# Optimization experiments

Hardware: AMD Instinct MI355X
Metric: run time of the kernel (lower is better)

## Reference

```python
import jax, jax.numpy as jnp
import numpy as np

R = 24  # voxel resolution
EPS = 0.0


def setup_inputs() -> dict:
    key = jax.random.key(0)
    pts = jax.random.normal(key, (32, 131072, 6), dtype=jnp.float32)
    return {"pts": pts}


def reference(pts):
    B, N, C = pts.shape
    coords = jax.lax.stop_gradient(pts[:, :, :3])            # [B,N,3] (detached in torch)
    feats = jnp.concatenate(
        [jnp.ones((B, N, 1), dtype=pts.dtype), pts[:, :, 3:]], axis=-1
    )                                                         # [B,N,4]

    # normalize coords into [0,1] per cloud
    nc = coords - coords.mean(axis=1, keepdims=True)          # [B,N,3]
    norm = jnp.linalg.norm(nc, axis=-1, keepdims=True)        # [B,N,1]
    max_norm = norm.max(axis=1, keepdims=True)                # [B,1,1]
    nc = nc / (max_norm * 2.0 + EPS) + 0.5

    nc = jnp.clip(nc * R, 0.0, R - 1)
    vox = jnp.round(nc).astype(jnp.int32)                     # [B,N,3]

    # flat voxel index with batch offset
    vidx = vox[..., 0] * R * R + vox[..., 1] * R + vox[..., 2]            # [B,N]
    flat_idx = (vidx + jnp.arange(B, dtype=jnp.int32)[:, None] * (R ** 3)).reshape(-1)

    F = feats.shape[-1]
    sums = jax.ops.segment_sum(feats.reshape(B * N, F), flat_idx,
                               num_segments=B * R ** 3)        # [B*R^3, F]
    cnts = jax.ops.segment_sum(jnp.ones((B * N,), dtype=pts.dtype), flat_idx,
                               num_segments=B * R ** 3)        # [B*R^3]
    avg = jnp.where(cnts[:, None] > 0, sums / jnp.maximum(cnts[:, None], 1.0), 0.0)

    out = avg.reshape(B, R, R, R, F)                           # [B,R,R,R,F]
    return jnp.transpose(out, (0, 4, 1, 2, 3))                 # [B,F,R,R,R]
```

## Files before the change

### kernel.cpp

```cpp
#include <hip/hip_runtime.h>

#define BATCH 32
#define NPTS 131072
#define RES 24
#define R3 (RES*RES*RES)
#define NCHUNK 8
#define CPTS (NPTS/NCHUNK)
#define NBLK_PER_B 64
#define MCHUNK (NPTS/NBLK_PER_B)
#define NSCAT (BATCH*NCHUNK)

#define QSCALE 128.0f
#define QBIAS 1024

#define WS_PARTIAL 0
#define WS_MEAN    49152
#define WS_MAXSQ   49920
#define WS_ACCUM   65536
#define PRIV_BYTES ((size_t)NSCAT * R3 * sizeof(unsigned long long))
#define SHARED_BYTES ((size_t)BATCH * R3 * 2 * sizeof(unsigned long long))

__global__ __launch_bounds__(256) void k_mean(const float* __restrict__ pts,
                                              double* __restrict__ partial) {
    int blk = blockIdx.x;
    int b = blk >> 6, c = blk & 63;
    const float4* base = (const float4*)(pts + ((size_t)b * NPTS + (size_t)c * MCHUNK) * 6);
    double s0 = 0, s1 = 0, s2 = 0;
    for (int i = threadIdx.x; i < MCHUNK / 2; i += 256) {
        float4 v0 = base[(size_t)i * 3];
        float4 v1 = base[(size_t)i * 3 + 1];
        float4 v2 = base[(size_t)i * 3 + 2];
        s0 += (double)v0.x + (double)v1.z;
        s1 += (double)v0.y + (double)v1.w;
        s2 += (double)v0.z + (double)v2.x;
    }
    for (int off = 32; off; off >>= 1) {
        s0 += __shfl_down(s0, off);
        s1 += __shfl_down(s1, off);
        s2 += __shfl_down(s2, off);
    }
    __shared__ double sh[4][3];
    int lane = threadIdx.x & 63, w = threadIdx.x >> 6;
    if (lane == 0) { sh[w][0] = s0; sh[w][1] = s1; sh[w][2] = s2; }
    __syncthreads();
    if (threadIdx.x == 0) {
        double t0 = 0, t1 = 0, t2 = 0;
        for (int q = 0; q < 4; q++) { t0 += sh[q][0]; t1 += sh[q][1]; t2 += sh[q][2]; }
        partial[(size_t)blk * 3 + 0] = t0;
        partial[(size_t)blk * 3 + 1] = t1;
        partial[(size_t)blk * 3 + 2] = t2;
    }
}

__global__ __launch_bounds__(64) void k_meanred(const double* __restrict__ partial,
                                                double* __restrict__ mean) {
    int b = threadIdx.x;
    if (b >= BATCH) return;
    double t0 = 0, t1 = 0, t2 = 0;
    for (int c = 0; c < NBLK_PER_B; c++) {
        const double* p = partial + ((size_t)b * NBLK_PER_B + c) * 3;
        t0 += p[0]; t1 += p[1]; t2 += p[2];
    }
    mean[b * 3 + 0] = t0 / (double)NPTS;
    mean[b * 3 + 1] = t1 / (double)NPTS;
    mean[b * 3 + 2] = t2 / (double)NPTS;
}

__global__ __launch_bounds__(256) void k_max(const float* __restrict__ pts,
                                             const double* __restrict__ mean,
                                             unsigned long long* __restrict__ maxsq) {
    int blk = blockIdx.x;
    int b = blk >> 6, c = blk & 63;
    double mx = mean[b * 3], my = mean[b * 3 + 1], mz = mean[b * 3 + 2];
    const float4* base = (const float4*)(pts + ((size_t)b * NPTS + (size_t)c * MCHUNK) * 6);
    double m = 0.0;
    for (int i = threadIdx.x; i < MCHUNK / 2; i += 256) {
        float4 v0 = base[(size_t)i * 3];
        float4 v1 = base[(size_t)i * 3 + 1];
        float4 v2 = base[(size_t)i * 3 + 2];
        double dx = (double)v0.x - mx, dy = (double)v0.y - my, dz = (double)v0.z - mz;
        m = fmax(m, dx * dx + dy * dy + dz * dz);
        dx = (double)v1.z - mx; dy = (double)v1.w - my; dz = (double)v2.x - mz;
        m = fmax(m, dx * dx + dy * dy + dz * dz);
    }
    for (int off = 32; off; off >>= 1)
        m = fmax(m, __shfl_down(m, off));
    __shared__ double sh[4];
    int lane = threadIdx.x & 63, w = threadIdx.x >> 6;
    if (lane == 0) sh[w] = m;
    __syncthreads();
    if (threadIdx.x == 0) {
        double t = fmax(fmax(sh[0], sh[1]), fmax(sh[2], sh[3]));
        atomicMax(&maxsq[b], (unsigned long long)__double_as_longlong(t));
    }
}

template <bool ATOMIC>
__global__ __launch_bounds__(1024, 4) void k_scatter_lds(const float* __restrict__ pts,
                                                         const double* __restrict__ mean,
                                                         const unsigned long long* __restrict__ maxsq,
                                                         unsigned long long* __restrict__ accum) {
    __shared__ unsigned long long acc[R3];
    int blk = blockIdx.x;
    int b = blk >> 3;
    int ch = blk & 7;
    for (int c = threadIdx.x; c < R3; c += 1024)
        acc[c] = 0ull;
    __syncthreads();

    double mx = mean[b * 3], my = mean[b * 3 + 1], mz = mean[b * 3 + 2];
    double inv = 1.0 / (2.0 * sqrt(__longlong_as_double((long long)maxsq[b])));

    const float4* base = (const float4*)(pts + ((size_t)b * NPTS + (size_t)ch * CPTS) * 6);

    auto point = [&](float x, float y, float z, float f1, float f2, float f3) {
        double vx = fma((double)x - mx, inv, 0.5) * 24.0;
        double vy = fma((double)y - my, inv, 0.5) * 24.0;
        double vz = fma((double)z - mz, inv, 0.5) * 24.0;
        vx = fmin(fmax(vx, 0.0), 23.0);
        vy = fmin(fmax(vy, 0.0), 23.0);
        vz = fmin(fmax(vz, 0.0), 23.0);
        int qx = (int)rint(vx);
        int qy = (int)rint(vy);
        int qz = (int)rint(vz);
        int cell = qx * (RES * RES) + qy * RES + qz;
        unsigned q1 = (unsigned)((int)rintf(f1 * QSCALE) + QBIAS);
        unsigned q2 = (unsigned)((int)rintf(f2 * QSCALE) + QBIAS);
        unsigned q3 = (unsigned)((int)rintf(f3 * QSCALE) + QBIAS);
        unsigned long long v = 1ull | ((unsigned long long)q1 << 10)
                                    | ((unsigned long long)q2 << 28)
                                    | ((unsigned long long)q3 << 46);
        atomicAdd(&acc[cell], v);
    };

    for (int it = 0; it < 2; ++it) {
        int pr = it * 4096 + threadIdx.x;
        float4 a0 = base[(size_t)pr * 3];
        float4 a1 = base[(size_t)pr * 3 + 1];
        float4 a2 = base[(size_t)pr * 3 + 2];
        float4 b0 = base[(size_t)(pr + 1024) * 3];
        float4 b1 = base[(size_t)(pr + 1024) * 3 + 1];
        float4 b2 = base[(size_t)(pr + 1024) * 3 + 2];
        float4 c0 = base[(size_t)(pr + 2048) * 3];
        float4 c1 = base[(size_t)(pr + 2048) * 3 + 1];
        float4 c2 = base[(size_t)(pr + 2048) * 3 + 2];
        float4 d0 = base[(size_t)(pr + 3072) * 3];
        float4 d1 = base[(size_t)(pr + 3072) * 3 + 1];
        float4 d2 = base[(size_t)(pr + 3072) * 3 + 2];
        point(a0.x, a0.y, a0.z, a0.w, a1.x, a1.y);
        point(a1.z, a1.w, a2.x, a2.y, a2.z, a2.w);
        point(b0.x, b0.y, b0.z, b0.w, b1.x, b1.y);
        point(b1.z, b1.w, b2.x, b2.y, b2.z, b2.w);
        point(c0.x, c0.y, c0.z, c0.w, c1.x, c1.y);
        point(c1.z, c1.w, c2.x, c2.y, c2.z, c2.w);
        point(d0.x, d0.y, d0.z, d0.w, d1.x, d1.y);
        point(d1.z, d1.w, d2.x, d2.y, d2.z, d2.w);
    }
    __syncthreads();

    if (ATOMIC) {
        for (int c = threadIdx.x; c < R3; c += 1024) {
            unsigned long long v = acc[c];
            if (v != 0ull) {
                unsigned long long cnt = v & 1023ull;
                unsigned long long g1 = (v >> 10) & 0x3FFFFull;
                unsigned long long g2 = (v >> 28) & 0x3FFFFull;
                unsigned long long g3 = (v >> 46);
                atomicAdd(&accum[((size_t)b * R3 + c) * 2 + 0], cnt | (g1 << 32));
                atomicAdd(&accum[((size_t)b * R3 + c) * 2 + 1], g2 | (g3 << 32));
            }
        }
    } else {
        ulonglong2* gacc = (ulonglong2*)(accum + (size_t)blk * R3);
        const ulonglong2* lacc = (const ulonglong2*)acc;
        for (int c = threadIdx.x; c < R3 / 2; c += 1024)
            gacc[c] = lacc[c];
    }
}

__device__ __forceinline__ void decode_write(long long cnt, long long s1, long long s2,
                                             long long s3, float* out, size_t obase) {
    if (cnt > 0) {
        float invc = 1.0f / (QSCALE * (float)cnt);
        out[obase]          = 1.0f;
        out[obase + R3]     = (float)(s1 - cnt * QBIAS) * invc;
        out[obase + 2 * R3] = (float)(s2 - cnt * QBIAS) * invc;
        out[obase + 3 * R3] = (float)(s3 - cnt * QBIAS) * invc;
    } else {
        out[obase]          = 0.0f;
        out[obase + R3]     = 0.0f;
        out[obase + 2 * R3] = 0.0f;
        out[obase + 3 * R3] = 0.0f;
    }
}

__global__ __launch_bounds__(256) void k_final_priv(const unsigned long long* __restrict__ accum,
                                                    float* __restrict__ out) {
    int cell = blockIdx.x * 256 + threadIdx.x;
    int b = cell / R3;
    int r = cell - b * R3;
    long long cnt = 0, s1 = 0, s2 = 0, s3 = 0;
    #pragma unroll
    for (int ch = 0; ch < NCHUNK; ch++) {
        unsigned long long v = accum[(size_t)(b * NCHUNK + ch) * R3 + r];
        cnt += (long long)(v & 1023ull);
        s1  += (long long)((v >> 10) & 0x3FFFFull);
        s2  += (long long)((v >> 28) & 0x3FFFFull);
        s3  += (long long)(v >> 46);
    }
    decode_write(cnt, s1, s2, s3, out, (size_t)b * 4 * R3 + r);
}

__global__ __launch_bounds__(256) void k_final_sum(const unsigned long long* __restrict__ accum,
                                                   float* __restrict__ out) {
    int cell = blockIdx.x * 256 + threadIdx.x;
    const ulonglong2 v = ((const ulonglong2*)accum)[cell];
    int b = cell / R3;
    int r = cell - b * R3;
    long long cnt = (long long)(v.x & 0xffffffffull);
    long long s1 = (long long)(v.x >> 32);
    long long s2 = (long long)(v.y & 0xffffffffull);
    long long s3 = (long long)(v.y >> 32);
    decode_write(cnt, s1, s2, s3, out, (size_t)b * 4 * R3 + r);
}

extern "C" void kernel_launch(void* const* d_in, const int* in_sizes, int n_in,
                              void* d_out, int out_size, void* d_ws, size_t ws_size,
                              hipStream_t stream) {
    const float* pts = (const float*)d_in[0];
    float* out = (float*)d_out;
    char* ws = (char*)d_ws;
    double* partial = (double*)(ws + WS_PARTIAL);
    double* mean = (double*)(ws + WS_MEAN);
    unsigned long long* maxsq = (unsigned long long*)(ws + WS_MAXSQ);
    unsigned long long* accum = (unsigned long long*)(ws + WS_ACCUM);
    bool priv = ws_size >= (size_t)WS_ACCUM + PRIV_BYTES;

    if (priv) {
        hipMemsetAsync(ws + WS_MAXSQ, 0, BATCH * sizeof(unsigned long long), stream);
    } else {
        hipMemsetAsync(ws + WS_MAXSQ, 0, (WS_ACCUM - WS_MAXSQ) + SHARED_BYTES, stream);
    }

    k_mean<<<BATCH * NBLK_PER_B, 256, 0, stream>>>(pts, partial);
    k_meanred<<<1, 64, 0, stream>>>(partial, mean);
    k_max<<<BATCH * NBLK_PER_B, 256, 0, stream>>>(pts, mean, maxsq);
    if (priv) {
        k_scatter_lds<false><<<NSCAT, 1024, 0, stream>>>(pts, mean, maxsq, accum);
        k_final_priv<<<(BATCH * R3) / 256, 256, 0, stream>>>(accum, out);
    } else {
        k_scatter_lds<true><<<NSCAT, 1024, 0, stream>>>(pts, mean, maxsq, accum);
        k_final_sum<<<(BATCH * R3) / 256, 256, 0, stream>>>(accum, out);
    }
}
```

Before: 78.51 us.

## Fuse mean, max, scatter and finalize into one cooperative kernel

Replaces the five-launch pipeline (mean, mean reduce, max, LDS scatter, finalize) with a single cooperative kernel of 256 blocks of 1024 threads that uses grid-wide syncs between stages. Each block reads its own chunk of points for the mean, the max-norm and the scatter passes, so re-reads of the same chunk may hit in cache, and the kernel-launch gaps are removed. In exchange, the mean and max passes now run on 256 large blocks instead of 2048 small ones, which lowers parallelism, and the four grid syncs add overhead. The design also depends on all 256 blocks being resident at once.

```diff
diff --git a/kernel.cpp b/kernel.cpp
--- a/kernel.cpp
+++ b/kernel.cpp
@@ -1,4 +1,7 @@
 #include <hip/hip_runtime.h>
+#include <hip/hip_cooperative_groups.h>
+
+namespace cg = cooperative_groups;
 
 #define BATCH 32
 #define NPTS 131072
@@ -6,9 +9,10 @@
 #define R3 (RES*RES*RES)
 #define NCHUNK 8
 #define CPTS (NPTS/NCHUNK)
+#define NBLOCKS (BATCH*NCHUNK)
+#define CELLS_PER_BLK ((BATCH*R3)/NBLOCKS)
 #define NBLK_PER_B 64
 #define MCHUNK (NPTS/NBLK_PER_B)
-#define NSCAT (BATCH*NCHUNK)
 
 #define QSCALE 128.0f
 #define QBIAS 1024
@@ -17,8 +21,181 @@
 #define WS_MEAN    49152
 #define WS_MAXSQ   49920
 #define WS_ACCUM   65536
-#define PRIV_BYTES ((size_t)NSCAT * R3 * sizeof(unsigned long long))
+#define PRIV_BYTES ((size_t)NBLOCKS * R3 * sizeof(unsigned long long))
 #define SHARED_BYTES ((size_t)BATCH * R3 * 2 * sizeof(unsigned long long))
+
+__device__ __forceinline__ void decode_write(long long cnt, long long s1, long long s2,
+                                             long long s3, float* out, size_t obase) {
+    if (cnt > 0) {
+        float invc = 1.0f / (QSCALE * (float)cnt);
+        out[obase]          = 1.0f;
+        out[obase + R3]     = (float)(s1 - cnt * QBIAS) * invc;
+        out[obase + 2 * R3] = (float)(s2 - cnt * QBIAS) * invc;
+        out[obase + 3 * R3] = (float)(s3 - cnt * QBIAS) * invc;
+    } else {
+        out[obase]          = 0.0f;
+        out[obase + R3]     = 0.0f;
+        out[obase + 2 * R3] = 0.0f;
+        out[obase + 3 * R3] = 0.0f;
+    }
+}
+
+__global__ __launch_bounds__(1024, 4) void k_fused(const float* __restrict__ pts,
+                                                   double* __restrict__ partial,
+                                                   double* __restrict__ mean,
+                                                   unsigned long long* __restrict__ maxsq,
+                                                   unsigned long long* __restrict__ accum,
+                                                   float* __restrict__ out) {
+    __shared__ unsigned long long acc[R3];
+    __shared__ double shred[16][3];
+    cg::grid_group grid = cg::this_grid();
+
+    const int blk = blockIdx.x;
+    const int b = blk >> 3, ch = blk & 7;
+    const int tid = threadIdx.x;
+    const int lane = tid & 63, w = tid >> 6;
+    const float4* base = (const float4*)(pts + ((size_t)b * NPTS + (size_t)ch * CPTS) * 6);
+
+    {
+        double s0 = 0, s1 = 0, s2 = 0;
+        for (int it = 0; it < 8; ++it) {
+            int pr = it * 1024 + tid;
+            float4 v0 = base[(size_t)pr * 3];
+            float4 v1 = base[(size_t)pr * 3 + 1];
+            float4 v2 = base[(size_t)pr * 3 + 2];
+            s0 += (double)v0.x + (double)v1.z;
+            s1 += (double)v0.y + (double)v1.w;
+            s2 += (double)v0.z + (double)v2.x;
+        }
+        for (int off = 32; off; off >>= 1) {
+            s0 += __shfl_down(s0, off);
+            s1 += __shfl_down(s1, off);
+            s2 += __shfl_down(s2, off);
+        }
+        if (lane == 0) { shred[w][0] = s0; shred[w][1] = s1; shred[w][2] = s2; }
+        __syncthreads();
+        if (tid == 0) {
+            double t0 = 0, t1 = 0, t2 = 0;
+            for (int q = 0; q < 16; q++) { t0 += shred[q][0]; t1 += shred[q][1]; t2 += shred[q][2]; }
+            partial[blk * 3 + 0] = t0;
+            partial[blk * 3 + 1] = t1;
+            partial[blk * 3 + 2] = t2;
+        }
+    }
+    grid.sync();
+
+    if (tid == 0 && ch == 0) {
+        double t0 = 0, t1 = 0, t2 = 0;
+        for (int c = 0; c < NCHUNK; c++) {
+            const double* p = partial + (size_t)(b * NCHUNK + c) * 3;
+            t0 += p[0]; t1 += p[1]; t2 += p[2];
+        }
+        mean[b * 3 + 0] = t0 / (double)NPTS;
+        mean[b * 3 + 1] = t1 / (double)NPTS;
+        mean[b * 3 + 2] = t2 / (double)NPTS;
+    }
+    grid.sync();
+
+    const double mx = mean[b * 3], my = mean[b * 3 + 1], mz = mean[b * 3 + 2];
+
+    {
+        double m = 0.0;
+        for (int it = 0; it < 8; ++it) {
+            int pr = it * 1024 + tid;
+            float4 v0 = base[(size_t)pr * 3];
+            float4 v1 = base[(size_t)pr * 3 + 1];
+            float4 v2 = base[(size_t)pr * 3 + 2];
+            double dx = (double)v0.x - mx, dy = (double)v0.y - my, dz = (double)v0.z - mz;
+            m = fmax(m, dx * dx + dy * dy + dz * dz);
+            dx = (double)v1.z - mx; dy = (double)v1.w - my; dz = (double)v2.x - mz;
+            m = fmax(m, dx * dx + dy * dy + dz * dz);
+        }
+        for (int off = 32; off; off >>= 1)
+            m = fmax(m, __shfl_down(m, off));
+        if (lane == 0) shred[w][0] = m;
+        __syncthreads();
+        if (tid == 0) {
+            double t = shred[0][0];
+            for (int q = 1; q < 16; q++) t = fmax(t, shred[q][0]);
+            atomicMax(&maxsq[b], (unsigned long long)__double_as_longlong(t));
+        }
+    }
+    grid.sync();
+
+    {
+        const double inv = 1.0 / (2.0 * sqrt(__longlong_as_double((long long)maxsq[b])));
+        for (int c = tid; c < R3; c += 1024)
+            acc[c] = 0ull;
+        __syncthreads();
+
+        auto point = [&](float x, float y, float z, float f1, float f2, float f3) {
+            double vx = fma((double)x - mx, inv, 0.5) * 24.0;
+            double vy = fma((double)y - my, inv, 0.5) * 24.0;
+            double vz = fma((double)z - mz, inv, 0.5) * 24.0;
+            vx = fmin(fmax(vx, 0.0), 23.0);
+            vy = fmin(fmax(vy, 0.0), 23.0);
+            vz = fmin(fmax(vz, 0.0), 23.0);
+            int qx = (int)rint(vx);
+            int qy = (int)rint(vy);
+            int qz = (int)rint(vz);
+            int cell = qx * (RES * RES) + qy * RES + qz;
+            unsigned q1 = (unsigned)((int)rintf(f1 * QSCALE) + QBIAS);
+            unsigned q2 = (unsigned)((int)rintf(f2 * QSCALE) + QBIAS);
+            unsigned q3 = (unsigned)((int)rintf(f3 * QSCALE) + QBIAS);
+            unsigned long long v = 1ull | ((unsigned long long)q1 << 10)
+                                        | ((unsigned long long)q2 << 28)
+                                        | ((unsigned long long)q3 << 46);
+            atomicAdd(&acc[cell], v);
+        };
+
+        for (int it = 0; it < 2; ++it) {
+            int pr = it * 4096 + tid;
+            float4 a0 = base[(size_t)pr * 3];
+            float4 a1 = base[(size_t)pr * 3 + 1];
+            float4 a2 = base[(size_t)pr * 3 + 2];
+            float4 b0 = base[(size_t)(pr + 1024) * 3];
+            float4 b1 = base[(size_t)(pr + 1024) * 3 + 1];
+            float4 b2 = base[(size_t)(pr + 1024) * 3 + 2];
+            float4 c0 = base[(size_t)(pr + 2048) * 3];
+            float4 c1 = base[(size_t)(pr + 2048) * 3 + 1];
+            float4 c2 = base[(size_t)(pr + 2048) * 3 + 2];
+            float4 d0 = base[(size_t)(pr + 3072) * 3];
+            float4 d1 = base[(size_t)(pr + 3072) * 3 + 1];
+            float4 d2 = base[(size_t)(pr + 3072) * 3 + 2];
+            point(a0.x, a0.y, a0.z, a0.w, a1.x, a1.y);
+            point(a1.z, a1.w, a2.x, a2.y, a2.z, a2.w);
+            point(b0.x, b0.y, b0.z, b0.w, b1.x, b1.y);
+            point(b1.z, b1.w, b2.x, b2.y, b2.z, b2.w);
+            point(c0.x, c0.y, c0.z, c0.w, c1.x, c1.y);
+            point(c1.z, c1.w, c2.x, c2.y, c2.z, c2.w);
+            point(d0.x, d0.y, d0.z, d0.w, d1.x, d1.y);
+            point(d1.z, d1.w, d2.x, d2.y, d2.z, d2.w);
+        }
+        __syncthreads();
+
+        ulonglong2* gacc = (ulonglong2*)(accum + (size_t)blk * R3);
+        const ulonglong2* lacc = (const ulonglong2*)acc;
+        for (int c = tid; c < R3 / 2; c += 1024)
+            gacc[c] = lacc[c];
+    }
+    grid.sync();
+
+    for (int i = tid; i < CELLS_PER_BLK; i += 1024) {
+        int cell = blk * CELLS_PER_BLK + i;
+        int bb = cell / R3;
+        int r = cell - bb * R3;
+        long long cnt = 0, s1 = 0, s2 = 0, s3 = 0;
+        #pragma unroll
+        for (int c2 = 0; c2 < NCHUNK; c2++) {
+            unsigned long long v = accum[(size_t)(bb * NCHUNK + c2) * R3 + r];
+            cnt += (long long)(v & 1023ull);
+            s1  += (long long)((v >> 10) & 0x3FFFFull);
+            s2  += (long long)((v >> 28) & 0x3FFFFull);
+            s3  += (long long)(v >> 46);
+        }
+        decode_write(cnt, s1, s2, s3, out, (size_t)bb * 4 * R3 + r);
+    }
+}
 
 __global__ __launch_bounds__(256) void k_mean(const float* __restrict__ pts,
                                               double* __restrict__ partial) {
@@ -95,11 +272,10 @@
     }
 }
 
-template <bool ATOMIC>
-__global__ __launch_bounds__(1024, 4) void k_scatter_lds(const float* __restrict__ pts,
-                                                         const double* __restrict__ mean,
-                                                         const unsigned long long* __restrict__ maxsq,
-                                                         unsigned long long* __restrict__ accum) {
+__global__ __launch_bounds__(1024, 4) void k_scatter_atomic(const float* __restrict__ pts,
+                                                            const double* __restrict__ mean,
+                                                            const unsigned long long* __restrict__ maxsq,
+                                                            unsigned long long* __restrict__ accum) {
     __shared__ unsigned long long acc[R3];
     int blk = blockIdx.x;
     int b = blk >> 3;
@@ -110,7 +286,6 @@
 
     double mx = mean[b * 3], my = mean[b * 3 + 1], mz = mean[b * 3 + 2];
     double inv = 1.0 / (2.0 * sqrt(__longlong_as_double((long long)maxsq[b])));
-
     const float4* base = (const float4*)(pts + ((size_t)b * NPTS + (size_t)ch * CPTS) * 6);
 
     auto point = [&](float x, float y, float z, float f1, float f2, float f3) {
@@ -158,57 +333,17 @@
     }
     __syncthreads();
 
-    if (ATOMIC) {
-        for (int c = threadIdx.x; c < R3; c += 1024) {
-            unsigned long long v = acc[c];
-            if (v != 0ull) {
-                unsigned long long cnt = v & 1023ull;
-                unsigned long long g1 = (v >> 10) & 0x3FFFFull;
-                unsigned long long g2 = (v >> 28) & 0x3FFFFull;
-                unsigned long long g3 = (v >> 46);
-                atomicAdd(&accum[((size_t)b * R3 + c) * 2 + 0], cnt | (g1 << 32));
-                atomicAdd(&accum[((size_t)b * R3 + c) * 2 + 1], g2 | (g3 << 32));
-            }
-        }
-    } else {
-        ulonglong2* gacc = (ulonglong2*)(accum + (size_t)blk * R3);
-        const ulonglong2* lacc = (const ulonglong2*)acc;
-        for (int c = threadIdx.x; c < R3 / 2; c += 1024)
-            gacc[c] = lacc[c];
-    }
-}
-
-__device__ __forceinline__ void decode_write(long long cnt, long long s1, long long s2,
-                                             long long s3, float* out, size_t obase) {
-    if (cnt > 0) {
-        float invc = 1.0f / (QSCALE * (float)cnt);
-        out[obase]          = 1.0f;
-        out[obase + R3]     = (float)(s1 - cnt * QBIAS) * invc;
-        out[obase + 2 * R3] = (float)(s2 - cnt * QBIAS) * invc;
-        out[obase + 3 * R3] = (float)(s3 - cnt * QBIAS) * invc;
-    } else {
-        out[obase]          = 0.0f;
-        out[obase + R3]     = 0.0f;
-        out[obase + 2 * R3] = 0.0f;
-        out[obase + 3 * R3] = 0.0f;
-    }
-}
-
-__global__ __launch_bounds__(256) void k_final_priv(const unsigned long long* __restrict__ accum,
-                                                    float* __restrict__ out) {
-    int cell = blockIdx.x * 256 + threadIdx.x;
-    int b = cell / R3;
-    int r = cell - b * R3;
-    long long cnt = 0, s1 = 0, s2 = 0, s3 = 0;
-    #pragma unroll
-    for (int ch = 0; ch < NCHUNK; ch++) {
-        unsigned long long v = accum[(size_t)(b * NCHUNK + ch) * R3 + r];
-        cnt += (long long)(v & 1023ull);
-        s1  += (long long)((v >> 10) & 0x3FFFFull);
-        s2  += (long long)((v >> 28) & 0x3FFFFull);
-        s3  += (long long)(v >> 46);
-    }
-    decode_write(cnt, s1, s2, s3, out, (size_t)b * 4 * R3 + r);
+    for (int c = threadIdx.x; c < R3; c += 1024) {
+        unsigned long long v = acc[c];
+        if (v != 0ull) {
+            unsigned long long cnt = v & 1023ull;
+            unsigned long long g1 = (v >> 10) & 0x3FFFFull;
+            unsigned long long g2 = (v >> 28) & 0x3FFFFull;
+            unsigned long long g3 = (v >> 46);
+            atomicAdd(&accum[((size_t)b * R3 + c) * 2 + 0], cnt | (g1 << 32));
+            atomicAdd(&accum[((size_t)b * R3 + c) * 2 + 1], g2 | (g3 << 32));
+        }
+    }
 }
 
 __global__ __launch_bounds__(256) void k_final_sum(const unsigned long long* __restrict__ accum,
@@ -238,18 +373,16 @@
 
     if (priv) {
         hipMemsetAsync(ws + WS_MAXSQ, 0, BATCH * sizeof(unsigned long long), stream);
+        void* args[] = {(void*)&pts, (void*)&partial, (void*)&mean,
+                        (void*)&maxsq, (void*)&accum, (void*)&out};
+        hipLaunchCooperativeKernel((const void*)k_fused, dim3(NBLOCKS), dim3(1024),
+                                   args, 0, stream);
     } else {
         hipMemsetAsync(ws + WS_MAXSQ, 0, (WS_ACCUM - WS_MAXSQ) + SHARED_BYTES, stream);
-    }
-
-    k_mean<<<BATCH * NBLK_PER_B, 256, 0, stream>>>(pts, partial);
-    k_meanred<<<1, 64, 0, stream>>>(partial, mean);
-    k_max<<<BATCH * NBLK_PER_B, 256, 0, stream>>>(pts, mean, maxsq);
-    if (priv) {
-        k_scatter_lds<false><<<NSCAT, 1024, 0, stream>>>(pts, mean, maxsq, accum);
-        k_final_priv<<<(BATCH * R3) / 256, 256, 0, stream>>>(accum, out);
-    } else {
-        k_scatter_lds<true><<<NSCAT, 1024, 0, stream>>>(pts, mean, maxsq, accum);
+        k_mean<<<BATCH * NBLK_PER_B, 256, 0, stream>>>(pts, partial);
+        k_meanred<<<1, 64, 0, stream>>>(partial, mean);
+        k_max<<<BATCH * NBLK_PER_B, 256, 0, stream>>>(pts, mean, maxsq);
+        k_scatter_atomic<<<NBLOCKS, 1024, 0, stream>>>(pts, mean, maxsq, accum);
         k_final_sum<<<(BATCH * R3) / 256, 256, 0, stream>>>(accum, out);
     }
 }
```

Result: slower. 182.3 us (+132.1%).
